# Kernel tuning notes

Measured on AMD Instinct MI355X. Metric: run time of the kernel, lower is better.

Reference implementation:

```python
import jax, jax.numpy as jnp
import numpy as np

NUM_EXPERTS = 8


def setup_inputs() -> dict:
    key = jax.random.key(0)
    k1, k2 = jax.random.split(key)
    G, T, D, E = 4, 2048, 1024, NUM_EXPERTS
    token_inputs = jax.random.normal(k1, (G, T, D), dtype=jnp.float32)
    router_weight = jax.random.normal(k2, (E, D), dtype=jnp.float32) * 0.02
    router_bias = jnp.zeros((E,), dtype=jnp.float32)
    return {
        "token_inputs": token_inputs,
        "router_weight": router_weight,
        "router_bias": router_bias,
        "expert_capacity": 320,
    }


def _routing(probs, expert_capacities):
    """Experts-preferred assignment: experts pick tokens in order, each up to
    its capacity, from tokens not yet taken by earlier experts."""
    G, T, E = probs.shape
    max_cap = max(expert_capacities)
    dispatch = jnp.zeros((G, T, E, max_cap), dtype=jnp.int32)
    combine = jnp.zeros((G, T, E, max_cap), dtype=probs.dtype)
    available = jnp.ones((G, T), dtype=probs.dtype)  # 1 if token unassigned
    g_idx = jnp.arange(G)[:, None]
    for e, cap in enumerate(expert_capacities):  # static small loop over experts
        masked = probs[:, :, e] * available                 # [G, T]
        gate, idx = jax.lax.top_k(masked, cap)              # [G, cap]
        c_idx = jnp.arange(cap)[None, :]
        dispatch = dispatch.at[g_idx, idx, e, c_idx].set(1)
        combine = combine.at[g_idx, idx, e, c_idx].set(gate)
        available = available.at[g_idx, idx].set(0.0)       # chosen tokens now taken
    return dispatch, combine


def reference(token_inputs, router_weight, router_bias, expert_capacity):
    x = token_inputs.astype(jnp.float32)
    # router logits: [G, T, E]
    logits = jnp.einsum("gtd,ed->gte", x, router_weight) + router_bias
    probs = jax.nn.softmax(logits, axis=-1)
    capacities = [int(expert_capacity)] * NUM_EXPERTS
    dispatch_mask, combine_array = _routing(probs, capacities)
    # router z-loss: mean over groups*tokens of logsumexp(logits)^2
    log_z = jax.nn.logsumexp(logits, axis=-1)
    z_loss = jnp.sum(log_z ** 2) / (logits.shape[0] * logits.shape[1])
    auxiliary_loss = jnp.float32(0.0)
    router_causal_loss = jnp.float32(0.0)
    return dispatch_mask, combine_array, auxiliary_loss, z_loss, router_causal_loss
```

## Files before the change

### kernel.cpp

```cpp
#include <hip/hip_runtime.h>

#define NEXP 8
#define NBLK 256
#define NTHR 1024

typedef unsigned long long u64;
typedef unsigned int u32;

union __align__(16) Smem {
    struct { float wl[NEXP * 1024]; double zred[16]; } a;
    struct { u64 keys[2048]; int part[NTHR]; } b;
    struct { int avail[2048]; int cnt[32]; int cnt2[32]; } c;
};

__global__ __launch_bounds__(NTHR, 4) void moe_router_kernel(
    const float* __restrict__ x,
    const float* __restrict__ w,
    const float* __restrict__ bias,
    float* __restrict__ out,
    float* __restrict__ probsT,
    u64* __restrict__ skey,
    double* __restrict__ zpart,
    int* __restrict__ bar,
    long long nout4, long long GT, int T, int G, int cap)
{
    __shared__ Smem sm;
    const int b = blockIdx.x;
    const int tid = threadIdx.x;
    const int lane = tid & 63;
    const int wv = tid >> 6;

    for (int i = tid; i < NEXP * 1024 / 4; i += NTHR)
        reinterpret_cast<float4*>(sm.a.wl)[i] = reinterpret_cast<const float4*>(w)[i];
    __syncthreads();

    {
        const float4 z = make_float4(0.f, 0.f, 0.f, 0.f);
        for (long long k = (long long)b * NTHR + tid; k < nout4; k += (long long)NBLK * NTHR)
            reinterpret_cast<float4*>(out)[k] = z;
    }

    {
        double zacc = 0.0;
#pragma unroll
        for (int s = 0; s < 2; ++s) {
            const long long t = (long long)b * 32 + wv * 2 + s;
            const float* xr = x + t * 1024;
            float acc[NEXP];
#pragma unroll
            for (int e = 0; e < NEXP; ++e) acc[e] = 0.f;
#pragma unroll
            for (int c = 0; c < 4; ++c) {
                const float4 xv = reinterpret_cast<const float4*>(xr)[c * 64 + lane];
#pragma unroll
                for (int e = 0; e < NEXP; ++e) {
                    const float4 wv4 = reinterpret_cast<const float4*>(sm.a.wl + e * 1024)[c * 64 + lane];
                    acc[e] = fmaf(xv.x, wv4.x, acc[e]);
                    acc[e] = fmaf(xv.y, wv4.y, acc[e]);
                    acc[e] = fmaf(xv.z, wv4.z, acc[e]);
                    acc[e] = fmaf(xv.w, wv4.w, acc[e]);
                }
            }
#pragma unroll
            for (int e = 0; e < NEXP; ++e) {
#pragma unroll
                for (int off = 32; off; off >>= 1) acc[e] += __shfl_xor(acc[e], off, 64);
            }
            if (lane == 0) {
                double l[NEXP]; double mx = -1e300;
#pragma unroll
                for (int e = 0; e < NEXP; ++e) { l[e] = (double)acc[e] + (double)bias[e]; mx = fmax(mx, l[e]); }
                double ex[NEXP]; double ssum = 0.0;
#pragma unroll
                for (int e = 0; e < NEXP; ++e) { ex[e] = exp(l[e] - mx); ssum += ex[e]; }
                const double inv = 1.0 / ssum;
#pragma unroll
                for (int e = 0; e < NEXP; ++e) probsT[(long long)e * GT + t] = (float)(ex[e] * inv);
                const double lse = mx + log(ssum);
                zacc += lse * lse;
            }
        }
        if (lane == 0) sm.a.zred[wv] = zacc;
    }
    __syncthreads();
    if (tid == 0) {
        double s = 0.0;
#pragma unroll
        for (int i = 0; i < 16; ++i) s += sm.a.zred[i];
        zpart[b] = s;
    }

    __syncthreads();
    if (tid == 0) {
        __threadfence();
        atomicAdd(&bar[0], 1);
        while (__hip_atomic_load(&bar[0], __ATOMIC_RELAXED, __HIP_MEMORY_SCOPE_AGENT) < NBLK)
            __builtin_amdgcn_s_sleep(2);
        __threadfence();
    }
    __syncthreads();

    {
        const int pair = b >> 3;
        const int sub  = b & 7;
        const int e = pair / G;
        const int g = pair - e * G;
        const float* p = probsT + (long long)e * GT + (long long)g * T;
        for (int j = tid; j < 2048; j += NTHR)
            sm.b.keys[j] = ((u64)__float_as_uint(p[j]) << 32) | (u32)(~(u32)j);
        __syncthreads();
        const int slot = tid & 255;
        const int q = tid >> 8;
        const u64 kt = sm.b.keys[sub * 256 + slot];
        const ulonglong2* k2 = reinterpret_cast<const ulonglong2*>(sm.b.keys) + q * 256;
        int r = 0;
#pragma unroll 8
        for (int j = 0; j < 256; ++j) {
            const ulonglong2 v = k2[j];
            r += (v.x > kt); r += (v.y > kt);
        }
        sm.b.part[tid] = r;
        __syncthreads();
        if (tid < 256) {
            const int rank = sm.b.part[tid] + sm.b.part[tid + 256] + sm.b.part[tid + 512] + sm.b.part[tid + 768];
            skey[(long long)pair * T + rank] = sm.b.keys[sub * 256 + tid];
        }
    }

    __syncthreads();
    if (b >= G) {
        if (tid == 0) { __threadfence(); atomicAdd(&bar[1], 1); }
        return;
    }
    if (tid == 0) {
        __threadfence();
        atomicAdd(&bar[1], 1);
        while (__hip_atomic_load(&bar[1], __ATOMIC_RELAXED, __HIP_MEMORY_SCOPE_AGENT) < NBLK)
            __builtin_amdgcn_s_sleep(2);
        __threadfence();
    }
    __syncthreads();

    const int g = b;
    u64 ka[NEXP], kb[NEXP];
#pragma unroll
    for (int e = 0; e < NEXP; ++e) {
        const long long base = (long long)(e * G + g) * T;
        ka[e] = skey[base + tid];
        kb[e] = skey[base + tid + 1024];
    }
    sm.c.avail[tid] = 1;
    sm.c.avail[tid + 1024] = 1;

    float* dispatch = out;
    float* combine  = out + GT * (long long)NEXP * cap;
    const long long gbase = (long long)g * T;
    const u64 lmask = (lane == 0) ? 0ull : ((~0ull) >> (64 - lane));

    for (int e = 0; e < NEXP; ++e) {
        __syncthreads();
        const u64 k0 = ka[e], k1 = kb[e];
        const u32 idx0 = ~(u32)k0, idx1 = ~(u32)k1;
        const float v0 = __uint_as_float((u32)(k0 >> 32));
        const float v1 = __uint_as_float((u32)(k1 >> 32));
        const int f0 = sm.c.avail[idx0];
        const int f1 = sm.c.avail[idx1];
        const u64 m0 = __ballot(f0);
        const u64 m1 = __ballot(f1);
        if (lane == 0) { sm.c.cnt[wv] = __popcll(m0); sm.c.cnt[16 + wv] = __popcll(m1); }
        __syncthreads();
        int vi = (lane < 32) ? sm.c.cnt[lane] : 0;
#pragma unroll
        for (int o = 1; o < 32; o <<= 1) { const int t2 = __shfl_up(vi, o, 64); if (lane >= o) vi += t2; }
        const int off0 = wv ? __shfl(vi, wv - 1, 64) : 0;
        const int off1 = __shfl(vi, 15 + wv, 64);
        const int S    = __shfl(vi, 31, 64);
        const int pre0 = off0 + __popcll(m0 & lmask);
        const int pre1 = off1 + __popcll(m1 & lmask);
        const bool s0 = f0 && (pre0 < cap);
        const bool s1 = f1 && (pre1 < cap);
        if (s0) { const long long o_ = ((gbase + idx0) * NEXP + e) * (long long)cap + pre0; dispatch[o_] = 1.0f; combine[o_] = v0; }
        if (s1) { const long long o_ = ((gbase + idx1) * NEXP + e) * (long long)cap + pre1; dispatch[o_] = 1.0f; combine[o_] = v1; }
        if (S < cap) {
            const int u0 = 1 - sm.c.avail[tid];
            const int u1 = 1 - sm.c.avail[tid + 1024];
            const u64 n0 = __ballot(u0);
            const u64 n1 = __ballot(u1);
            if (lane == 0) { sm.c.cnt2[wv] = __popcll(n0); sm.c.cnt2[16 + wv] = __popcll(n1); }
            __syncthreads();
            int vj = (lane < 32) ? sm.c.cnt2[lane] : 0;
#pragma unroll
            for (int o = 1; o < 32; o <<= 1) { const int t2 = __shfl_up(vj, o, 64); if (lane >= o) vj += t2; }
            const int qoff0 = wv ? __shfl(vj, wv - 1, 64) : 0;
            const int qoff1 = __shfl(vj, 15 + wv, 64);
            const int q0 = qoff0 + __popcll(n0 & lmask);
            const int q1 = qoff1 + __popcll(n1 & lmask);
            const int nfill = cap - S;
            if (u0 && q0 < nfill) { const long long o_ = ((gbase + tid) * NEXP + e) * (long long)cap + S + q0; dispatch[o_] = 1.0f; }
            if (u1 && q1 < nfill) { const long long o_ = ((gbase + tid + 1024) * NEXP + e) * (long long)cap + S + q1; dispatch[o_] = 1.0f; }
        }
        if (s0) sm.c.avail[idx0] = 0;
        if (s1) sm.c.avail[idx1] = 0;
    }

    if (g == 0 && tid < 64) {
        double s = zpart[tid] + zpart[tid + 64] + zpart[tid + 128] + zpart[tid + 192];
#pragma unroll
        for (int o = 32; o; o >>= 1) s += __shfl_xor(s, o, 64);
        if (tid == 0) {
            float* sc = out + 2 * GT * (long long)NEXP * cap;
            sc[0] = 0.0f;
            sc[1] = (float)(s / (double)GT);
            sc[2] = 0.0f;
        }
    }
}

extern "C" void kernel_launch(void* const* d_in, const int* in_sizes, int n_in,
                              void* d_out, int out_size, void* d_ws, size_t ws_size,
                              hipStream_t stream) {
    (void)n_in; (void)ws_size;
    const float* x    = (const float*)d_in[0];
    const float* w    = (const float*)d_in[1];
    const float* bias = (const float*)d_in[2];

    const int E = in_sizes[2];
    const int D = in_sizes[1] / E;
    const long long GT = (long long)in_sizes[0] / D;
    const int T = 2048;
    const int G = (int)(GT / T);
    const int cap = (int)(((long long)out_size - 3) / (2 * GT * E));
    const long long nout4 = ((long long)out_size - 3) >> 2;

    int*    bar    = (int*)d_ws;
    double* zpart  = (double*)((char*)d_ws + 4096);
    float*  probsT = (float*)((char*)d_ws + 16384);
    u64*    skey   = (u64*)((char*)d_ws + 16384 + (size_t)E * GT * sizeof(float));

    hipMemsetAsync(bar, 0, 16, stream);

    moe_router_kernel<<<NBLK, NTHR, 0, stream>>>(
        x, w, bias, (float*)d_out, probsT, skey, zpart, bar,
        nout4, GT, T, G, cap);
}
```

Baseline: 87.62 us.

## Split router kernel into role-specialized blocks synchronized by per-group flags

Replaces the single persistent grid with its global barriers by a larger grid of specialized blocks: projection blocks, zero-fill blocks, ranking blocks and per-group routing blocks, which wait on per-group counters instead of grid-wide barriers. The routing blocks now stage selections in shared memory and write dispatch/combine only after the zero-fill completes, so the big output memset overlaps with projection and ranking. The design relies on spin-waiting blocks not starving producer blocks and adds a second scatter pass from shared memory.

```diff
diff --git a/kernel.cpp b/kernel.cpp
--- a/kernel.cpp
+++ b/kernel.cpp
@@ -1,19 +1,23 @@
 #include <hip/hip_runtime.h>
 
 #define NEXP 8
-#define NBLK 256
-#define NTHR 1024
+#define NPB 1024
+#define NFL 1788
+#define NRK 256
+#define MAXCAP 384
+#define NTHR 512
 
 typedef unsigned long long u64;
 typedef unsigned int u32;
 
 union __align__(16) Smem {
-    struct { float wl[NEXP * 1024]; double zred[16]; } a;
+    struct { float wl[NEXP * 1024]; double zred[8]; } a;
     struct { u64 keys[2048]; int part[NTHR]; } b;
-    struct { int avail[2048]; int cnt[32]; int cnt2[32]; } c;
+    struct { int avail[2048]; int cnt[32]; int cnt2[32];
+             u64 cbuf[NEXP * MAXCAP]; } c;
 };
 
-__global__ __launch_bounds__(NTHR, 4) void moe_router_kernel(
+__global__ __launch_bounds__(NTHR) void moe_fat_kernel(
     const float* __restrict__ x,
     const float* __restrict__ w,
     const float* __restrict__ bias,
@@ -21,8 +25,9 @@
     float* __restrict__ probsT,
     u64* __restrict__ skey,
     double* __restrict__ zpart,
-    int* __restrict__ bar,
-    long long nout4, long long GT, int T, int G, int cap)
+    int* __restrict__ flags,
+    long long nout4, int out_size,
+    long long GT, int T, int G, int cap)
 {
     __shared__ Smem sm;
     const int b = blockIdx.x;
@@ -30,81 +35,84 @@
     const int lane = tid & 63;
     const int wv = tid >> 6;
 
-    for (int i = tid; i < NEXP * 1024 / 4; i += NTHR)
-        reinterpret_cast<float4*>(sm.a.wl)[i] = reinterpret_cast<const float4*>(w)[i];
-    __syncthreads();
-
-    {
+    if (b < NPB) {
+        for (int i = tid; i < NEXP * 1024 / 4; i += NTHR)
+            reinterpret_cast<float4*>(sm.a.wl)[i] = reinterpret_cast<const float4*>(w)[i];
+        __syncthreads();
+
+        const long long t = (long long)b * 8 + wv;
+        const float* xr = x + t * 1024;
+        float acc[NEXP];
+#pragma unroll
+        for (int e = 0; e < NEXP; ++e) acc[e] = 0.f;
+#pragma unroll
+        for (int c = 0; c < 4; ++c) {
+            const int d = c * 256 + lane * 4;
+            const float4 xv = *reinterpret_cast<const float4*>(xr + d);
+#pragma unroll
+            for (int e = 0; e < NEXP; ++e) {
+                const float4 wv4 = *reinterpret_cast<const float4*>(sm.a.wl + e * 1024 + d);
+                acc[e] = fmaf(xv.x, wv4.x, acc[e]);
+                acc[e] = fmaf(xv.y, wv4.y, acc[e]);
+                acc[e] = fmaf(xv.z, wv4.z, acc[e]);
+                acc[e] = fmaf(xv.w, wv4.w, acc[e]);
+            }
+        }
+#pragma unroll
+        for (int e = 0; e < NEXP; ++e) {
+#pragma unroll
+            for (int off = 32; off; off >>= 1) acc[e] += __shfl_xor(acc[e], off, 64);
+        }
+        if (lane == 0) {
+            double l[NEXP]; double mx = -1e300;
+#pragma unroll
+            for (int e = 0; e < NEXP; ++e) { l[e] = (double)acc[e] + (double)bias[e]; mx = fmax(mx, l[e]); }
+            double ex[NEXP]; double s = 0.0;
+#pragma unroll
+            for (int e = 0; e < NEXP; ++e) { ex[e] = exp(l[e] - mx); s += ex[e]; }
+            const double inv = 1.0 / s;
+#pragma unroll
+            for (int e = 0; e < NEXP; ++e) probsT[(long long)e * GT + t] = (float)(ex[e] * inv);
+            const double lse = mx + log(s);
+            sm.a.zred[wv] = lse * lse;
+        }
+        __syncthreads();
+        if (tid == 0) {
+            double s = 0.0;
+#pragma unroll
+            for (int i = 0; i < 8; ++i) s += sm.a.zred[i];
+            zpart[b] = s;
+            __threadfence();
+            atomicAdd(&flags[b / (NPB / 4)], 1);
+        }
+        return;
+    }
+
+    if (b < NPB + NFL) {
+        const int fb = b - NPB;
+        const long long stride = (long long)NFL * NTHR;
         const float4 z = make_float4(0.f, 0.f, 0.f, 0.f);
-        for (long long k = (long long)b * NTHR + tid; k < nout4; k += (long long)NBLK * NTHR)
+        for (long long k = (long long)fb * NTHR + tid; k < nout4; k += stride)
             reinterpret_cast<float4*>(out)[k] = z;
-    }
-
-    {
-        double zacc = 0.0;
-#pragma unroll
-        for (int s = 0; s < 2; ++s) {
-            const long long t = (long long)b * 32 + wv * 2 + s;
-            const float* xr = x + t * 1024;
-            float acc[NEXP];
-#pragma unroll
-            for (int e = 0; e < NEXP; ++e) acc[e] = 0.f;
-#pragma unroll
-            for (int c = 0; c < 4; ++c) {
-                const float4 xv = reinterpret_cast<const float4*>(xr)[c * 64 + lane];
-#pragma unroll
-                for (int e = 0; e < NEXP; ++e) {
-                    const float4 wv4 = reinterpret_cast<const float4*>(sm.a.wl + e * 1024)[c * 64 + lane];
-                    acc[e] = fmaf(xv.x, wv4.x, acc[e]);
-                    acc[e] = fmaf(xv.y, wv4.y, acc[e]);
-                    acc[e] = fmaf(xv.z, wv4.z, acc[e]);
-                    acc[e] = fmaf(xv.w, wv4.w, acc[e]);
-                }
-            }
-#pragma unroll
-            for (int e = 0; e < NEXP; ++e) {
-#pragma unroll
-                for (int off = 32; off; off >>= 1) acc[e] += __shfl_xor(acc[e], off, 64);
-            }
-            if (lane == 0) {
-                double l[NEXP]; double mx = -1e300;
-#pragma unroll
-                for (int e = 0; e < NEXP; ++e) { l[e] = (double)acc[e] + (double)bias[e]; mx = fmax(mx, l[e]); }
-                double ex[NEXP]; double ssum = 0.0;
-#pragma unroll
-                for (int e = 0; e < NEXP; ++e) { ex[e] = exp(l[e] - mx); ssum += ex[e]; }
-                const double inv = 1.0 / ssum;
-#pragma unroll
-                for (int e = 0; e < NEXP; ++e) probsT[(long long)e * GT + t] = (float)(ex[e] * inv);
-                const double lse = mx + log(ssum);
-                zacc += lse * lse;
-            }
-        }
-        if (lane == 0) sm.a.zred[wv] = zacc;
-    }
-    __syncthreads();
-    if (tid == 0) {
-        double s = 0.0;
-#pragma unroll
-        for (int i = 0; i < 16; ++i) s += sm.a.zred[i];
-        zpart[b] = s;
-    }
-
-    __syncthreads();
-    if (tid == 0) {
-        __threadfence();
-        atomicAdd(&bar[0], 1);
-        while (__hip_atomic_load(&bar[0], __ATOMIC_RELAXED, __HIP_MEMORY_SCOPE_AGENT) < NBLK)
-            __builtin_amdgcn_s_sleep(2);
-        __threadfence();
-    }
-    __syncthreads();
-
-    {
-        const int pair = b >> 3;
-        const int sub  = b & 7;
+        __syncthreads();
+        if (tid == 0) { __threadfence(); atomicAdd(&flags[8], 1); }
+        return;
+    }
+
+    if (b < NPB + NFL + NRK) {
+        const int b3 = b - NPB - NFL;
+        const int pair = b3 >> 3;
+        const int sub  = b3 & 7;
         const int e = pair / G;
         const int g = pair - e * G;
+        const int ptgt = NPB / G;
+        if (tid == 0) {
+            while (__hip_atomic_load(&flags[g], __ATOMIC_RELAXED, __HIP_MEMORY_SCOPE_AGENT) < ptgt)
+                __builtin_amdgcn_s_sleep(2);
+            __threadfence();
+        }
+        __syncthreads();
+
         const float* p = probsT + (long long)e * GT + (long long)g * T;
         for (int j = tid; j < 2048; j += NTHR)
             sm.b.keys[j] = ((u64)__float_as_uint(p[j]) << 32) | (u32)(~(u32)j);
@@ -112,106 +120,134 @@
         const int slot = tid & 255;
         const int q = tid >> 8;
         const u64 kt = sm.b.keys[sub * 256 + slot];
-        const ulonglong2* k2 = reinterpret_cast<const ulonglong2*>(sm.b.keys) + q * 256;
+        const ulonglong2* k2 = reinterpret_cast<const ulonglong2*>(sm.b.keys) + q * 512;
         int r = 0;
 #pragma unroll 8
-        for (int j = 0; j < 256; ++j) {
+        for (int j = 0; j < 512; ++j) {
             const ulonglong2 v = k2[j];
             r += (v.x > kt); r += (v.y > kt);
         }
         sm.b.part[tid] = r;
         __syncthreads();
         if (tid < 256) {
-            const int rank = sm.b.part[tid] + sm.b.part[tid + 256] + sm.b.part[tid + 512] + sm.b.part[tid + 768];
+            const int rank = sm.b.part[tid] + sm.b.part[tid + 256];
             skey[(long long)pair * T + rank] = sm.b.keys[sub * 256 + tid];
         }
-    }
-
-    __syncthreads();
-    if (b >= G) {
-        if (tid == 0) { __threadfence(); atomicAdd(&bar[1], 1); }
+        __syncthreads();
+        if (tid == 0) { __threadfence(); atomicAdd(&flags[4 + g], 1); }
         return;
     }
+
+    const int g = b - NPB - NFL - NRK;
+    const int rtgt = NRK / 4;
     if (tid == 0) {
-        __threadfence();
-        atomicAdd(&bar[1], 1);
-        while (__hip_atomic_load(&bar[1], __ATOMIC_RELAXED, __HIP_MEMORY_SCOPE_AGENT) < NBLK)
+        while (__hip_atomic_load(&flags[4 + g], __ATOMIC_RELAXED, __HIP_MEMORY_SCOPE_AGENT) < rtgt)
             __builtin_amdgcn_s_sleep(2);
         __threadfence();
     }
     __syncthreads();
 
-    const int g = b;
-    u64 ka[NEXP], kb[NEXP];
-#pragma unroll
+    for (int j = tid; j < 2048; j += NTHR) sm.c.avail[j] = 1;
+    const u64 lmask = (lane == 0) ? 0ull : ((~0ull) >> (64 - lane));
+    const long long gbase = (long long)g * T;
+
     for (int e = 0; e < NEXP; ++e) {
-        const long long base = (long long)(e * G + g) * T;
-        ka[e] = skey[base + tid];
-        kb[e] = skey[base + tid + 1024];
-    }
-    sm.c.avail[tid] = 1;
-    sm.c.avail[tid + 1024] = 1;
+        const long long kb = (long long)(e * G + g) * T;
+        u64 k[4];
+#pragma unroll
+        for (int j = 0; j < 4; ++j) k[j] = skey[kb + tid + j * NTHR];
+        __syncthreads();
+        u32 idx[4]; int f[4]; u64 m[4];
+#pragma unroll
+        for (int j = 0; j < 4; ++j) {
+            idx[j] = ~(u32)k[j];
+            f[j] = sm.c.avail[idx[j]];
+            m[j] = __ballot(f[j]);
+            if (lane == 0) sm.c.cnt[wv + 8 * j] = __popcll(m[j]);
+        }
+        __syncthreads();
+        int vi = (lane < 32) ? sm.c.cnt[lane] : 0;
+#pragma unroll
+        for (int o = 1; o < 32; o <<= 1) { const int t2 = __shfl_up(vi, o, 64); if (lane >= o) vi += t2; }
+        const int S = __shfl(vi, 31, 64);
+        bool sel[4]; int pre[4];
+#pragma unroll
+        for (int j = 0; j < 4; ++j) {
+            const int seg = wv + 8 * j;
+            const int off = seg ? __shfl(vi, seg - 1, 64) : 0;
+            pre[j] = off + __popcll(m[j] & lmask);
+            sel[j] = f[j] && (pre[j] < cap);
+            if (sel[j]) sm.c.cbuf[e * cap + pre[j]] = ((k[j] >> 32) << 32) | (u64)idx[j];
+        }
+        if (S < cap) {
+            int u[4]; u64 n[4];
+#pragma unroll
+            for (int j = 0; j < 4; ++j) {
+                u[j] = 1 - sm.c.avail[tid + j * NTHR];
+                n[j] = __ballot(u[j]);
+                if (lane == 0) sm.c.cnt2[wv + 8 * j] = __popcll(n[j]);
+            }
+            __syncthreads();
+            int vj = (lane < 32) ? sm.c.cnt2[lane] : 0;
+#pragma unroll
+            for (int o = 1; o < 32; o <<= 1) { const int t2 = __shfl_up(vj, o, 64); if (lane >= o) vj += t2; }
+            const int nfill = cap - S;
+#pragma unroll
+            for (int j = 0; j < 4; ++j) {
+                const int seg = wv + 8 * j;
+                const int qoff = seg ? __shfl(vj, seg - 1, 64) : 0;
+                const int qj = qoff + __popcll(n[j] & lmask);
+                if (u[j] && qj < nfill) sm.c.cbuf[e * cap + S + qj] = (u64)(u32)(tid + j * NTHR);
+            }
+        }
+#pragma unroll
+        for (int j = 0; j < 4; ++j) if (sel[j]) sm.c.avail[idx[j]] = 0;
+    }
+    __syncthreads();
+
+    if (g == 0) {
+        if (tid == 0) {
+            const int ptgt = NPB / 4;
+#pragma unroll
+            for (int gg = 0; gg < 4; ++gg)
+                while (__hip_atomic_load(&flags[gg], __ATOMIC_RELAXED, __HIP_MEMORY_SCOPE_AGENT) < ptgt)
+                    __builtin_amdgcn_s_sleep(2);
+            __threadfence();
+        }
+        __syncthreads();
+        if (tid < 64) {
+            double s = 0.0;
+            for (int i = tid; i < NPB; i += 64) s += zpart[i];
+#pragma unroll
+            for (int o = 32; o; o >>= 1) s += __shfl_xor(s, o, 64);
+            if (tid == 0) {
+                float* sc = out + 2 * GT * (long long)NEXP * cap;
+                for (long long j = nout4 * 4; j < (long long)out_size - 3; ++j) out[j] = 0.f;
+                sc[0] = 0.0f;
+                sc[1] = (float)(s / (double)GT);
+                sc[2] = 0.0f;
+            }
+        }
+    }
+
+    if (tid == 0) {
+        while (__hip_atomic_load(&flags[8], __ATOMIC_RELAXED, __HIP_MEMORY_SCOPE_AGENT) < NFL)
+            __builtin_amdgcn_s_sleep(2);
+        __threadfence();
+    }
+    __syncthreads();
 
     float* dispatch = out;
     float* combine  = out + GT * (long long)NEXP * cap;
-    const long long gbase = (long long)g * T;
-    const u64 lmask = (lane == 0) ? 0ull : ((~0ull) >> (64 - lane));
-
+#pragma unroll
     for (int e = 0; e < NEXP; ++e) {
-        __syncthreads();
-        const u64 k0 = ka[e], k1 = kb[e];
-        const u32 idx0 = ~(u32)k0, idx1 = ~(u32)k1;
-        const float v0 = __uint_as_float((u32)(k0 >> 32));
-        const float v1 = __uint_as_float((u32)(k1 >> 32));
-        const int f0 = sm.c.avail[idx0];
-        const int f1 = sm.c.avail[idx1];
-        const u64 m0 = __ballot(f0);
-        const u64 m1 = __ballot(f1);
-        if (lane == 0) { sm.c.cnt[wv] = __popcll(m0); sm.c.cnt[16 + wv] = __popcll(m1); }
-        __syncthreads();
-        int vi = (lane < 32) ? sm.c.cnt[lane] : 0;
-#pragma unroll
-        for (int o = 1; o < 32; o <<= 1) { const int t2 = __shfl_up(vi, o, 64); if (lane >= o) vi += t2; }
-        const int off0 = wv ? __shfl(vi, wv - 1, 64) : 0;
-        const int off1 = __shfl(vi, 15 + wv, 64);
-        const int S    = __shfl(vi, 31, 64);
-        const int pre0 = off0 + __popcll(m0 & lmask);
-        const int pre1 = off1 + __popcll(m1 & lmask);
-        const bool s0 = f0 && (pre0 < cap);
-        const bool s1 = f1 && (pre1 < cap);
-        if (s0) { const long long o_ = ((gbase + idx0) * NEXP + e) * (long long)cap + pre0; dispatch[o_] = 1.0f; combine[o_] = v0; }
-        if (s1) { const long long o_ = ((gbase + idx1) * NEXP + e) * (long long)cap + pre1; dispatch[o_] = 1.0f; combine[o_] = v1; }
-        if (S < cap) {
-            const int u0 = 1 - sm.c.avail[tid];
-            const int u1 = 1 - sm.c.avail[tid + 1024];
-            const u64 n0 = __ballot(u0);
-            const u64 n1 = __ballot(u1);
-            if (lane == 0) { sm.c.cnt2[wv] = __popcll(n0); sm.c.cnt2[16 + wv] = __popcll(n1); }
-            __syncthreads();
-            int vj = (lane < 32) ? sm.c.cnt2[lane] : 0;
-#pragma unroll
-            for (int o = 1; o < 32; o <<= 1) { const int t2 = __shfl_up(vj, o, 64); if (lane >= o) vj += t2; }
-            const int qoff0 = wv ? __shfl(vj, wv - 1, 64) : 0;
-            const int qoff1 = __shfl(vj, 15 + wv, 64);
-            const int q0 = qoff0 + __popcll(n0 & lmask);
-            const int q1 = qoff1 + __popcll(n1 & lmask);
-            const int nfill = cap - S;
-            if (u0 && q0 < nfill) { const long long o_ = ((gbase + tid) * NEXP + e) * (long long)cap + S + q0; dispatch[o_] = 1.0f; }
-            if (u1 && q1 < nfill) { const long long o_ = ((gbase + tid + 1024) * NEXP + e) * (long long)cap + S + q1; dispatch[o_] = 1.0f; }
-        }
-        if (s0) sm.c.avail[idx0] = 0;
-        if (s1) sm.c.avail[idx1] = 0;
-    }
-
-    if (g == 0 && tid < 64) {
-        double s = zpart[tid] + zpart[tid + 64] + zpart[tid + 128] + zpart[tid + 192];
-#pragma unroll
-        for (int o = 32; o; o >>= 1) s += __shfl_xor(s, o, 64);
-        if (tid == 0) {
-            float* sc = out + 2 * GT * (long long)NEXP * cap;
-            sc[0] = 0.0f;
-            sc[1] = (float)(s / (double)GT);
-            sc[2] = 0.0f;
+        for (int c = tid; c < cap; c += NTHR) {
+            const u64 en = sm.c.cbuf[e * cap + c];
+            const u32 idx = (u32)en;
+            const float val = __uint_as_float((u32)(en >> 32));
+            const long long o_ = ((gbase + idx) * NEXP + e) * (long long)cap + c;
+            dispatch[o_] = 1.0f;
+            combine[o_]  = val;
         }
     }
 }
@@ -232,14 +268,14 @@
     const int cap = (int)(((long long)out_size - 3) / (2 * GT * E));
     const long long nout4 = ((long long)out_size - 3) >> 2;
 
-    int*    bar    = (int*)d_ws;
+    int*    flags  = (int*)d_ws;
     double* zpart  = (double*)((char*)d_ws + 4096);
     float*  probsT = (float*)((char*)d_ws + 16384);
     u64*    skey   = (u64*)((char*)d_ws + 16384 + (size_t)E * GT * sizeof(float));
 
-    hipMemsetAsync(bar, 0, 16, stream);
-
-    moe_router_kernel<<<NBLK, NTHR, 0, stream>>>(
-        x, w, bias, (float*)d_out, probsT, skey, zpart, bar,
-        nout4, GT, T, G, cap);
+    hipMemsetAsync(flags, 0, 64, stream);
+
+    moe_fat_kernel<<<NPB + NFL + NRK + G, NTHR, 0, stream>>>(
+        x, w, bias, (float*)d_out, probsT, skey, zpart, flags,
+        nout4, out_size, GT, T, G, cap);
 }
```

Result: slower. 191.9 us (+119.0%).
